# Kernel tuning notes

Hardware: AMD Instinct MI355X
Metric: run time of the kernel (lower is better)

The kernel has to match this reference:

```python
import jax, jax.numpy as jnp
import numpy as np

EMBED = 512
EXPAND = 1024


def setup_inputs() -> dict:
    key = jax.random.key(0)
    k1, k2, k3, k4, k5 = jax.random.split(key, 5)
    B, C, P, N = 4, EMBED, 16, 1024
    x = jax.random.normal(k1, (B, C, P, N), dtype=jnp.float32)
    # 1x1 conv weights == per-pixel linear maps over the channel dim
    Wqkv = jax.random.normal(k2, (1 + 2 * EXPAND, C), dtype=jnp.float32) * (1.0 / np.sqrt(C))
    bqkv = jax.random.normal(k3, (1 + 2 * EXPAND,), dtype=jnp.float32) * 0.01
    Wout = jax.random.normal(k4, (C, EXPAND), dtype=jnp.float32) * (1.0 / np.sqrt(EXPAND))
    bout = jax.random.normal(k5, (C,), dtype=jnp.float32) * 0.01
    return {"x": x, "Wqkv": Wqkv, "bqkv": bqkv, "Wout": Wout, "bout": bout}


def reference(x, Wqkv, bqkv, Wout, bout):
    # qkv 1x1 conv: (B,C,P,N) -> (B, 1+2E, P, N)
    qkv = jnp.einsum('oc,bcpn->bopn', Wqkv, x) + bqkv[None, :, None, None]
    E = EXPAND
    query = qkv[:, :1]            # (B,1,P,N)
    key_t = qkv[:, 1:1 + E]       # (B,E,P,N)
    value = qkv[:, 1 + E:]        # (B,E,P,N)
    # softmax over patches dim (last axis); attn_dropout p=0.0 -> identity
    context_scores = jax.nn.softmax(query, axis=-1)
    # weighted sum over N, keepdim -> (B,E,P,1)
    context_vector = jnp.sum(key_t * context_scores, axis=-1, keepdims=True)
    # broadcast gate
    out = jax.nn.relu(value) * context_vector  # (B,E,P,N)
    # out 1x1 conv back to embed channels
    out = jnp.einsum('oe,bepn->bopn', Wout, out) + bout[None, :, None, None]
    return out
```

## Files before the change

### kernel.cpp

```cpp
#include <hip/hip_runtime.h>

#define EMBED 512
#define EXPAND 1024
#define PNUM 16
#define NLEN 1024
#define CHW (PNUM * NLEN)
#define SLABS 64

typedef unsigned short u16;
typedef unsigned int u32;
typedef __bf16 bf16x8 __attribute__((ext_vector_type(8)));
typedef u16 u16x8 __attribute__((ext_vector_type(8)));
typedef float f32x4 __attribute__((ext_vector_type(4)));

__device__ __forceinline__ u16 f2bf(float f) {
  u32 u = __builtin_bit_cast(u32, f);
  return (u16)((u + 0x7FFFu + ((u >> 16) & 1u)) >> 16);
}
__device__ __forceinline__ float bf2f(u16 h) {
  return __builtin_bit_cast(float, (u32)h << 16);
}
__device__ __forceinline__ void gld16(const u16* g, u16* l) {
  __builtin_amdgcn_global_load_lds((__attribute__((address_space(1))) void*)g,
                                   (__attribute__((address_space(3))) void*)l,
                                   16, 0, 0);
}
__device__ __forceinline__ f32x4 MFMA(bf16x8 a, bf16x8 b, f32x4 c) {
  return __builtin_amdgcn_mfma_f32_16x16x32_bf16(a, b, c, 0, 0, 0);
}

__global__ __launch_bounds__(256) void k_convert_w(
    const float* __restrict__ Wqkv, const float* __restrict__ Wout,
    u16* __restrict__ WvB, u16* __restrict__ WoutB) {
  const int NV = EXPAND * EMBED;
  int idx = (blockIdx.x * 256 + threadIdx.x) * 4;
  if (idx < NV) {
    float4 v = *(const float4*)(Wqkv + (size_t)(1 + EXPAND) * EMBED + idx);
    uint2 u = make_uint2((u32)f2bf(v.x) | ((u32)f2bf(v.y) << 16),
                         (u32)f2bf(v.z) | ((u32)f2bf(v.w) << 16));
    *(uint2*)(WvB + idx) = u;
  } else {
    int j = idx - NV;
    float4 v = *(const float4*)(Wout + j);
    uint2 u = make_uint2((u32)f2bf(v.x) | ((u32)f2bf(v.y) << 16),
                         (u32)f2bf(v.z) | ((u32)f2bf(v.w) << 16));
    *(uint2*)(WoutB + j) = u;
  }
}

__global__ __launch_bounds__(256) void k_convert_x(
    const float* __restrict__ x, const float* __restrict__ Wqkv,
    float* __restrict__ qpart, u16* __restrict__ xbT) {
  __shared__ __align__(16) u16 tile[128 * 64];
  __shared__ float qp[256 * 4];
  const int slab = blockIdx.x >> 4;
  const int nw = (blockIdx.x >> 1) & 7;
  const int chalf = blockIdx.x & 1;
  const int b = slab >> 4, p = slab & 15;
  const int t = threadIdx.x;
  const int c8 = t & 7;
  const int ng = t >> 3;
  const float* xs = x + (size_t)b * (EMBED * CHW) + (size_t)p * NLEN + nw * 128;
  u16* dst = xbT + (size_t)slab * (NLEN * EMBED) + (size_t)(nw * 128) * EMBED;
  float qa[4] = {0.f, 0.f, 0.f, 0.f};

  for (int cc = 0; cc < 4; ++cc) {
    const int cbase = chalf * 256 + cc * 64;
    float4 v[8];
#pragma unroll
    for (int k = 0; k < 8; ++k)
      v[k] = *(const float4*)(xs + (size_t)(cbase + c8 * 8 + k) * CHW + ng * 4);
    const float* w0 = Wqkv + cbase + c8 * 8;
#pragma unroll
    for (int k = 0; k < 8; ++k) {
      qa[0] += w0[k] * v[k].x;
      qa[1] += w0[k] * v[k].y;
      qa[2] += w0[k] * v[k].z;
      qa[3] += w0[k] * v[k].w;
    }
#pragma unroll
    for (int j = 0; j < 4; ++j) {
      const int nl = ng * 4 + j;
      float e[8];
#pragma unroll
      for (int k = 0; k < 8; ++k)
        e[k] = (j == 0) ? v[k].x : (j == 1) ? v[k].y : (j == 2) ? v[k].z : v[k].w;
      uint4 pk;
      pk.x = (u32)f2bf(e[0]) | ((u32)f2bf(e[1]) << 16);
      pk.y = (u32)f2bf(e[2]) | ((u32)f2bf(e[3]) << 16);
      pk.z = (u32)f2bf(e[4]) | ((u32)f2bf(e[5]) << 16);
      pk.w = (u32)f2bf(e[6]) | ((u32)f2bf(e[7]) << 16);
      *(uint4*)(tile + nl * 64 + ((c8 ^ (nl & 7)) << 3)) = pk;
    }
    __syncthreads();
#pragma unroll
    for (int m = 0; m < 4; ++m) {
      const int s = m * 256 + t;
      const int nl = s >> 3, ch = s & 7;
      uint4 vv = *(const uint4*)(tile + nl * 64 + ((ch ^ (nl & 7)) << 3));
      *(uint4*)(dst + (size_t)nl * EMBED + cbase + ch * 8) = vv;
    }
    __syncthreads();
  }
  qp[t * 4 + 0] = qa[0];
  qp[t * 4 + 1] = qa[1];
  qp[t * 4 + 2] = qa[2];
  qp[t * 4 + 3] = qa[3];
  __syncthreads();
  if (t < 128) {
    float a = 0.f;
#pragma unroll
    for (int o = 0; o < 8; ++o) a += qp[((((t >> 2) << 3) + o) << 2) + (t & 3)];
    qpart[(size_t)slab * 2048 + chalf * 1024 + nw * 128 + t] = a;
  }
}

__global__ __launch_bounds__(256) void k_attn1(
    const float* __restrict__ qpart, const u16* __restrict__ xbT,
    float* __restrict__ ypart) {
  __shared__ float red[4];
  __shared__ float sm[128];
  __shared__ float yp[4][512];
  const int slab = blockIdx.x >> 3, n8 = blockIdx.x & 7;
  const int t = threadIdx.x, w = t >> 6, l = t & 63;
  const float* q0 = qpart + (size_t)slab * 2048;
  const float* q1 = q0 + 1024;

  float4 qa = ((const float4*)q0)[t];
  float4 qb = ((const float4*)q1)[t];
  float4 q4 = make_float4(qa.x + qb.x, qa.y + qb.y, qa.z + qb.z, qa.w + qb.w);
  float m = fmaxf(fmaxf(q4.x, q4.y), fmaxf(q4.z, q4.w));
#pragma unroll
  for (int sh = 32; sh; sh >>= 1) m = fmaxf(m, __shfl_xor(m, sh, 64));
  if (l == 0) red[w] = m;
  __syncthreads();
  float gm = fmaxf(fmaxf(red[0], red[1]), fmaxf(red[2], red[3]));
  float s = __expf(q4.x - gm) + __expf(q4.y - gm) + __expf(q4.z - gm) + __expf(q4.w - gm);
#pragma unroll
  for (int sh = 32; sh; sh >>= 1) s += __shfl_xor(s, sh, 64);
  __syncthreads();
  if (l == 0) red[w] = s;
  __syncthreads();
  float gs = red[0] + red[1] + red[2] + red[3];
  if (t < 128) {
    const int n = n8 * 128 + t;
    sm[t] = __expf(q0[n] + q1[n] - gm) / gs;
  }
  __syncthreads();

  float ya[8] = {0.f, 0.f, 0.f, 0.f, 0.f, 0.f, 0.f, 0.f};
  const u16* xs = xbT + (size_t)slab * (NLEN * EMBED) + (size_t)(n8 * 128) * EMBED;
  for (int ni = 0; ni < 32; ++ni) {
    const int nloc = ni * 4 + w;
    const float sc = sm[nloc];
    u16x8 v = *(const u16x8*)(xs + (size_t)nloc * EMBED + l * 8);
#pragma unroll
    for (int j = 0; j < 8; ++j) ya[j] += sc * bf2f(v[j]);
  }
#pragma unroll
  for (int j = 0; j < 8; ++j) yp[w][l * 8 + j] = ya[j];
  __syncthreads();
  for (int c = t; c < 512; c += 256)
    ypart[((size_t)slab * 8 + n8) * 512 + c] = yp[0][c] + yp[1][c] + yp[2][c] + yp[3][c];
}

__global__ __launch_bounds__(256) void k_attn2(
    const float* __restrict__ ypart, const float* __restrict__ Wqkv,
    const float* __restrict__ bqkv, float* __restrict__ cv) {
  __shared__ float yl[512];
  const int slab = blockIdx.x >> 2, ec = blockIdx.x & 3;
  const int t = threadIdx.x;
  const int e = ec * 256 + t;
  const float* yb = ypart + (size_t)slab * 8 * 512;
  for (int c = t; c < 512; c += 256) {
    float a = 0.f;
#pragma unroll
    for (int k = 0; k < 8; ++k) a += yb[k * 512 + c];
    yl[c] = a;
  }
  __syncthreads();
  const float* wk = Wqkv + (size_t)(1 + e) * EMBED;
  float a = 0.f;
#pragma unroll 4
  for (int c0 = 0; c0 < EMBED; c0 += 4) {
    float4 wv = *(const float4*)(wk + c0);
    a += wv.x * yl[c0] + wv.y * yl[c0 + 1] + wv.z * yl[c0 + 2] + wv.w * yl[c0 + 3];
  }
  cv[(size_t)slab * EXPAND + e] = a + bqkv[1 + e];
}

template <int K, int NT>
__device__ __forceinline__ void gemm128(const u16* __restrict__ Abase,
                                        const u16* __restrict__ Bbase,
                                        u16* lds, f32x4 (&acc)[4][4]) {
  const int t = threadIdx.x;
  const int w = t >> 6, l = t & 63;
  const int wr = w >> 1, wc = w & 1;
  const int lr = l & 15, lj = l >> 4;

#pragma unroll 1
  for (int kt = 0; kt < NT; ++kt) {
    const int kc0 = kt * 64;
#pragma unroll
    for (int i = 0; i < 4; ++i) {
      const int s = i * 256 + t;
      const int row = s >> 3, pch = s & 7;
      const int gch = (pch ^ (row & 7)) << 3;
      gld16(Abase + (size_t)row * K + kc0 + gch, lds + s * 8);
      gld16(Bbase + (size_t)row * K + kc0 + gch, lds + 8192 + s * 8);
    }
    __syncthreads();
    bf16x8 af[4][2], bg[4][2];
#pragma unroll
    for (int mi = 0; mi < 4; ++mi)
#pragma unroll
      for (int kc = 0; kc < 2; ++kc) {
        const int row = wr * 64 + mi * 16 + lr;
        af[mi][kc] = *(const bf16x8*)(lds + row * 64 +
                                      (((kc * 4 + lj) ^ (row & 7)) << 3));
      }
#pragma unroll
    for (int ni = 0; ni < 4; ++ni)
#pragma unroll
      for (int kc = 0; kc < 2; ++kc) {
        const int row = wc * 64 + ni * 16 + lr;
        bg[ni][kc] = *(const bf16x8*)(lds + 8192 + row * 64 +
                                      (((kc * 4 + lj) ^ (row & 7)) << 3));
      }
#pragma unroll
    for (int mi = 0; mi < 4; ++mi)
#pragma unroll
      for (int ni = 0; ni < 4; ++ni)
#pragma unroll
        for (int kc = 0; kc < 2; ++kc)
          acc[mi][ni] = MFMA(af[mi][kc], bg[ni][kc], acc[mi][ni]);
    __syncthreads();
  }
}

__global__ __launch_bounds__(256, 4) void k_gemm1(
    const u16* __restrict__ xbT, const u16* __restrict__ WvB,
    const float* __restrict__ bqkv, const float* __restrict__ cv,
    u16* __restrict__ midT) {
  __shared__ __align__(16) u16 lds[16384];
  const int bid = blockIdx.x;
  const int xc = bid & 7, k = bid >> 3;
  const int te = k & 7;
  const int gg = ((k >> 3) << 3) | xc;
  const int slab = gg >> 3, tn = gg & 7;
  const u16* A = xbT + (size_t)slab * (NLEN * EMBED) + (size_t)tn * 128 * EMBED;
  const u16* B = WvB + (size_t)te * 128 * EMBED;
  f32x4 acc[4][4];
  const f32x4 z = {0.f, 0.f, 0.f, 0.f};
#pragma unroll
  for (int i = 0; i < 4; ++i)
#pragma unroll
    for (int j = 0; j < 4; ++j) acc[i][j] = z;
  gemm128<EMBED, 8>(A, B, lds, acc);

  const int t = threadIdx.x, w = t >> 6, l = t & 63;
  const int wr = w >> 1, wc = w & 1;
  const int lr = l & 15, lq4 = (l >> 4) * 4;
#pragma unroll
  for (int ni = 0; ni < 4; ++ni) {
    const int col = wc * 64 + ni * 16 + lr;
    const int e = te * 128 + col;
    const float bv = bqkv[1 + EXPAND + e];
    const float cve = cv[(size_t)slab * EXPAND + e];
#pragma unroll
    for (int mi = 0; mi < 4; ++mi) {
      const int nr = wr * 64 + mi * 16 + lq4;
#pragma unroll
      for (int r = 0; r < 4; ++r) {
        float v = acc[mi][ni][r] + bv;
        v = v > 0.f ? v * cve : 0.f;
        const int row = nr + r;
        lds[row * 128 + ((((col >> 3) ^ (row & 7)) << 3) | (col & 7))] = f2bf(v);
      }
    }
  }
  __syncthreads();
  u16* mt = midT + (size_t)slab * (NLEN * EXPAND) + (size_t)te * 128;
#pragma unroll
  for (int it = 0; it < 8; ++it) {
    const int row = w * 32 + it * 4 + (l >> 4);
    const int ch = (l & 15) ^ (row & 7);
    uint4 v = *(const uint4*)(lds + row * 128 + ch * 8);
    *(uint4*)(mt + (size_t)(tn * 128 + row) * EXPAND + (l & 15) * 8) = v;
  }
}

__global__ __launch_bounds__(256, 4) void k_gemm2(
    const u16* __restrict__ midT, const u16* __restrict__ WoutB,
    const float* __restrict__ bout, float* __restrict__ out) {
  __shared__ __align__(16) u16 lds[16384];
  const int bid = blockIdx.x;
  const int xc = bid & 7, k = bid >> 3;
  const int to = k & 3;
  const int gg = ((k >> 2) << 3) | xc;
  const int slab = gg >> 3, tn = gg & 7;
  const int b = slab >> 4, p = slab & 15;
  const u16* A = midT + (size_t)slab * (NLEN * EXPAND) + (size_t)tn * 128 * EXPAND;
  const u16* B = WoutB + (size_t)to * 128 * EXPAND;
  f32x4 acc[4][4];
  const f32x4 z = {0.f, 0.f, 0.f, 0.f};
#pragma unroll
  for (int i = 0; i < 4; ++i)
#pragma unroll
    for (int j = 0; j < 4; ++j) acc[i][j] = z;
  gemm128<EXPAND, 16>(A, B, lds, acc);

  const int t = threadIdx.x, w = t >> 6, l = t & 63;
  const int wr = w >> 1, wc = w & 1;
  const int lr = l & 15, lq4 = (l >> 4) * 4;
  float* ob = out + (size_t)b * (EMBED * CHW) + (size_t)p * NLEN;
#pragma unroll
  for (int ni = 0; ni < 4; ++ni) {
    const int o = to * 128 + wc * 64 + ni * 16 + lr;
    const float bo = bout[o];
#pragma unroll
    for (int mi = 0; mi < 4; ++mi) {
      const int nr = tn * 128 + wr * 64 + mi * 16 + lq4;
      float4 v;
      v.x = acc[mi][ni][0] + bo;
      v.y = acc[mi][ni][1] + bo;
      v.z = acc[mi][ni][2] + bo;
      v.w = acc[mi][ni][3] + bo;
      *(float4*)(ob + (size_t)o * CHW + nr) = v;
    }
  }
}

extern "C" void kernel_launch(void* const* d_in, const int* in_sizes, int n_in,
                              void* d_out, int out_size, void* d_ws, size_t ws_size,
                              hipStream_t stream) {
  const float* x = (const float*)d_in[0];
  const float* Wqkv = (const float*)d_in[1];
  const float* bqkv = (const float*)d_in[2];
  const float* Wout = (const float*)d_in[3];
  const float* bout = (const float*)d_in[4];
  float* out = (float*)d_out;

  char* ws = (char*)d_ws;
  u16* xbT = (u16*)ws;
  u16* WvB = (u16*)(ws + 67108864);
  u16* WoutB = (u16*)(ws + 68157440);
  float* cv = (float*)(ws + 69468160);
  u16* midT = (u16*)(ws + 69730304);
  float* ypart = (float*)(ws + 69730304);
  float* qpart = (float*)(ws + 69730304 + 1048576);

  k_convert_w<<<1024, 256, 0, stream>>>(Wqkv, Wout, WvB, WoutB);
  k_convert_x<<<1024, 256, 0, stream>>>(x, Wqkv, qpart, xbT);
  k_attn1<<<512, 256, 0, stream>>>(qpart, xbT, ypart);
  k_attn2<<<256, 256, 0, stream>>>(ypart, Wqkv, bqkv, cv);
  k_gemm1<<<4096, 256, 0, stream>>>(xbT, WvB, bqkv, cv, midT);
  k_gemm2<<<2048, 256, 0, stream>>>(midT, WoutB, bout, out);
}
```

Before: 260.6 us.

## Merge weight and input conversion kernels; retile output GEMM to 256x128 blocks

The two conversion kernels become one launch: extra blocks past the first 1024 do the bf16 weight conversion. This saves one kernel launch and lets the two jobs run at the same time. The output GEMM now uses 512-thread blocks that each compute a 256x128 tile, so every loaded Wout tile is shared by twice as many rows and the weight traffic drops. The shared gemm128 helper is replaced by an inline single-buffered loop with two barriers per K step. That may lose any load/compute overlap the helper had, and the larger LDS footprint may lower occupancy.

```diff
diff --git a/kernel.cpp b/kernel.cpp
--- a/kernel.cpp
+++ b/kernel.cpp
@@ -29,35 +29,34 @@
   return __builtin_amdgcn_mfma_f32_16x16x32_bf16(a, b, c, 0, 0, 0);
 }
 
-__global__ __launch_bounds__(256) void k_convert_w(
-    const float* __restrict__ Wqkv, const float* __restrict__ Wout,
-    u16* __restrict__ WvB, u16* __restrict__ WoutB) {
-  const int NV = EXPAND * EMBED;
-  int idx = (blockIdx.x * 256 + threadIdx.x) * 4;
-  if (idx < NV) {
-    float4 v = *(const float4*)(Wqkv + (size_t)(1 + EXPAND) * EMBED + idx);
-    uint2 u = make_uint2((u32)f2bf(v.x) | ((u32)f2bf(v.y) << 16),
-                         (u32)f2bf(v.z) | ((u32)f2bf(v.w) << 16));
-    *(uint2*)(WvB + idx) = u;
-  } else {
-    int j = idx - NV;
-    float4 v = *(const float4*)(Wout + j);
-    uint2 u = make_uint2((u32)f2bf(v.x) | ((u32)f2bf(v.y) << 16),
-                         (u32)f2bf(v.z) | ((u32)f2bf(v.w) << 16));
-    *(uint2*)(WoutB + j) = u;
-  }
-}
-
-__global__ __launch_bounds__(256) void k_convert_x(
+__global__ __launch_bounds__(256) void k_convert_xw(
     const float* __restrict__ x, const float* __restrict__ Wqkv,
-    float* __restrict__ qpart, u16* __restrict__ xbT) {
+    const float* __restrict__ Wout, float* __restrict__ qpart,
+    u16* __restrict__ xbT, u16* __restrict__ WvB, u16* __restrict__ WoutB) {
   __shared__ __align__(16) u16 tile[128 * 64];
   __shared__ float qp[256 * 4];
+  const int t = threadIdx.x;
+  if (blockIdx.x >= 1024) {
+    const int NV = EXPAND * EMBED;
+    int idx = ((blockIdx.x - 1024) * 256 + t) * 4;
+    if (idx < NV) {
+      float4 v = *(const float4*)(Wqkv + (size_t)(1 + EXPAND) * EMBED + idx);
+      uint2 u = make_uint2((u32)f2bf(v.x) | ((u32)f2bf(v.y) << 16),
+                           (u32)f2bf(v.z) | ((u32)f2bf(v.w) << 16));
+      *(uint2*)(WvB + idx) = u;
+    } else {
+      int j = idx - NV;
+      float4 v = *(const float4*)(Wout + j);
+      uint2 u = make_uint2((u32)f2bf(v.x) | ((u32)f2bf(v.y) << 16),
+                           (u32)f2bf(v.z) | ((u32)f2bf(v.w) << 16));
+      *(uint2*)(WoutB + j) = u;
+    }
+    return;
+  }
   const int slab = blockIdx.x >> 4;
   const int nw = (blockIdx.x >> 1) & 7;
   const int chalf = blockIdx.x & 1;
   const int b = slab >> 4, p = slab & 15;
-  const int t = threadIdx.x;
   const int c8 = t & 7;
   const int ng = t >> 3;
   const float* xs = x + (size_t)b * (EMBED * CHW) + (size_t)p * NLEN + nw * 128;
@@ -290,29 +289,73 @@
   }
 }
 
-__global__ __launch_bounds__(256, 4) void k_gemm2(
+__global__ __launch_bounds__(512, 4) void k_gemm2(
     const u16* __restrict__ midT, const u16* __restrict__ WoutB,
     const float* __restrict__ bout, float* __restrict__ out) {
-  __shared__ __align__(16) u16 lds[16384];
+  __shared__ __align__(16) u16 lds[24576];
   const int bid = blockIdx.x;
   const int xc = bid & 7, k = bid >> 3;
   const int to = k & 3;
   const int gg = ((k >> 2) << 3) | xc;
-  const int slab = gg >> 3, tn = gg & 7;
+  const int slab = gg >> 2, tn = gg & 3;
   const int b = slab >> 4, p = slab & 15;
-  const u16* A = midT + (size_t)slab * (NLEN * EXPAND) + (size_t)tn * 128 * EXPAND;
+  const u16* A = midT + (size_t)slab * (NLEN * EXPAND) + (size_t)tn * 256 * EXPAND;
   const u16* B = WoutB + (size_t)to * 128 * EXPAND;
+  const int t = threadIdx.x, w = t >> 6, l = t & 63;
+  const int wr = w >> 1, wc = w & 1;
+  const int lr = l & 15, lj = l >> 4, lq4 = (l >> 4) * 4;
   f32x4 acc[4][4];
   const f32x4 z = {0.f, 0.f, 0.f, 0.f};
 #pragma unroll
   for (int i = 0; i < 4; ++i)
 #pragma unroll
     for (int j = 0; j < 4; ++j) acc[i][j] = z;
-  gemm128<EXPAND, 16>(A, B, lds, acc);
-
-  const int t = threadIdx.x, w = t >> 6, l = t & 63;
-  const int wr = w >> 1, wc = w & 1;
-  const int lr = l & 15, lq4 = (l >> 4) * 4;
+
+#pragma unroll 1
+  for (int kt = 0; kt < 16; ++kt) {
+    const int kc0 = kt * 64;
+#pragma unroll
+    for (int i = 0; i < 4; ++i) {
+      const int s = i * 512 + t;
+      const int row = s >> 3, pch = s & 7;
+      gld16(A + (size_t)row * EXPAND + kc0 + ((pch ^ (row & 7)) << 3),
+            lds + s * 8);
+    }
+#pragma unroll
+    for (int i = 0; i < 2; ++i) {
+      const int s = i * 512 + t;
+      const int row = s >> 3, pch = s & 7;
+      gld16(B + (size_t)row * EXPAND + kc0 + ((pch ^ (row & 7)) << 3),
+            lds + 16384 + s * 8);
+    }
+    __syncthreads();
+    bf16x8 af[4][2], bg[4][2];
+#pragma unroll
+    for (int mi = 0; mi < 4; ++mi)
+#pragma unroll
+      for (int kc = 0; kc < 2; ++kc) {
+        const int row = wr * 64 + mi * 16 + lr;
+        af[mi][kc] = *(const bf16x8*)(lds + row * 64 +
+                                      (((kc * 4 + lj) ^ (row & 7)) << 3));
+      }
+#pragma unroll
+    for (int ni = 0; ni < 4; ++ni)
+#pragma unroll
+      for (int kc = 0; kc < 2; ++kc) {
+        const int row = wc * 64 + ni * 16 + lr;
+        bg[ni][kc] = *(const bf16x8*)(lds + 16384 + row * 64 +
+                                      (((kc * 4 + lj) ^ (row & 7)) << 3));
+      }
+#pragma unroll
+    for (int mi = 0; mi < 4; ++mi)
+#pragma unroll
+      for (int ni = 0; ni < 4; ++ni)
+#pragma unroll
+        for (int kc = 0; kc < 2; ++kc)
+          acc[mi][ni] = MFMA(af[mi][kc], bg[ni][kc], acc[mi][ni]);
+    __syncthreads();
+  }
+
   float* ob = out + (size_t)b * (EMBED * CHW) + (size_t)p * NLEN;
 #pragma unroll
   for (int ni = 0; ni < 4; ++ni) {
@@ -320,7 +363,7 @@
     const float bo = bout[o];
 #pragma unroll
     for (int mi = 0; mi < 4; ++mi) {
-      const int nr = tn * 128 + wr * 64 + mi * 16 + lq4;
+      const int nr = tn * 256 + wr * 64 + mi * 16 + lq4;
       float4 v;
       v.x = acc[mi][ni][0] + bo;
       v.y = acc[mi][ni][1] + bo;
@@ -350,10 +393,9 @@
   float* ypart = (float*)(ws + 69730304);
   float* qpart = (float*)(ws + 69730304 + 1048576);
 
-  k_convert_w<<<1024, 256, 0, stream>>>(Wqkv, Wout, WvB, WoutB);
-  k_convert_x<<<1024, 256, 0, stream>>>(x, Wqkv, qpart, xbT);
+  k_convert_xw<<<2048, 256, 0, stream>>>(x, Wqkv, Wout, qpart, xbT, WvB, WoutB);
   k_attn1<<<512, 256, 0, stream>>>(qpart, xbT, ypart);
   k_attn2<<<256, 256, 0, stream>>>(ypart, Wqkv, bqkv, cv);
   k_gemm1<<<4096, 256, 0, stream>>>(xbT, WvB, bqkv, cv, midT);
-  k_gemm2<<<2048, 256, 0, stream>>>(midT, WoutB, bout, out);
-}
+  k_gemm2<<<1024, 512, 0, stream>>>(midT, WoutB, bout, out);
+}
```

Result: faster. 252.9 us (median of 2 runs) (-3.0%).
